# Performance work log

Measured on AMD Instinct MI355X. Metric: run time of the kernel, lower is better.

The kernel has to match this reference:

```python
import jax, jax.numpy as jnp
import numpy as np

B, L, D = 2, 2048, 2048
H, G, HD = 16, 4, 128
EPS = 1e-6
THETA_BASE = 10000.0


def setup_inputs() -> dict:
    key = jax.random.key(0)
    ks = jax.random.split(key, 5)
    x = jax.random.normal(ks[0], (B, L, D), jnp.float32)
    Wq = jax.random.normal(ks[1], (D, H * HD), jnp.float32) * 0.02
    Wk = jax.random.normal(ks[2], (D, G * HD), jnp.float32) * 0.02
    Wv = jax.random.normal(ks[3], (D, G * HD), jnp.float32) * 0.02
    Wo = jax.random.normal(ks[4], (H * HD, D), jnp.float32) * 0.02
    q_scale = jnp.ones((HD,), jnp.float32)
    k_scale = jnp.ones((HD,), jnp.float32)
    # Well-formed RoPE tables of shape [L, HD] (duplicated-half layout expected by apply_rope)
    inv_freq = 1.0 / (THETA_BASE ** (jnp.arange(0, HD // 2, dtype=jnp.float32) * 2.0 / HD))  # [HD/2]
    angles = jnp.arange(L, dtype=jnp.float32)[:, None] * inv_freq[None, :]  # [L, HD/2]
    angles = jnp.concatenate([angles, angles], axis=1)  # [L, HD]
    cos = jnp.cos(angles)
    sin = jnp.sin(angles)
    # Causal mask: True = masked (matches masked_fill(mask, -inf))
    mask = jnp.triu(jnp.ones((L, L), dtype=bool), k=1)
    return {"x": x, "Wq": Wq, "Wk": Wk, "Wv": Wv, "Wo": Wo,
            "q_scale": q_scale, "k_scale": k_scale, "cos": cos, "sin": sin, "mask": mask}


def _rmsnorm(x, scale):
    var = jnp.mean(x * x, axis=-1, keepdims=True)
    return x * jax.lax.rsqrt(var + EPS) * scale


def _rope(x, cos, sin):
    # x: [B, h, L, HD]; cos/sin: [L, HD]
    hd = x.shape[-1]
    x1, x2 = x[..., : hd // 2], x[..., hd // 2 :]
    rotated = jnp.concatenate([-x2, x1], axis=-1)
    return x * cos[None, None] + rotated * sin[None, None]


def reference(x, Wq, Wk, Wv, Wo, q_scale, k_scale, cos, sin, mask):
    b, l, _ = x.shape
    q = (x @ Wq).reshape(b, l, H, HD).transpose(0, 2, 1, 3)  # [B,H,L,HD]
    k = (x @ Wk).reshape(b, l, G, HD).transpose(0, 2, 1, 3)  # [B,G,L,HD]
    v = (x @ Wv).reshape(b, l, G, HD).transpose(0, 2, 1, 3)
    q = _rmsnorm(q, q_scale)
    k = _rmsnorm(k, k_scale)
    q = _rope(q, cos, sin)
    k = _rope(k, cos, sin)
    gs = H // G
    k = jnp.repeat(k, gs, axis=1)  # [B,H,L,HD]
    v = jnp.repeat(v, gs, axis=1)
    scores = jnp.einsum('bhqd,bhkd->bhqk', q, k)
    scores = jnp.where(mask, -jnp.inf, scores)
    # NB: faithful to the source's unusual scaling by head_dim**2 (not sqrt)
    w = jax.nn.softmax(scores / float(HD ** 2), axis=-1)
    out = jnp.einsum('bhqk,bhkd->bhqd', w, v).transpose(0, 2, 1, 3).reshape(b, l, H * HD)
    return out @ Wo
```

## Files before the change

kernel.cpp:

```cpp
#include <hip/hip_runtime.h>
#include <math.h>

#define SEQ 2048
#define DMODEL 2048
#define NHQ 16
#define NHK 4

typedef __attribute__((ext_vector_type(8))) short short8;
typedef __attribute__((ext_vector_type(4))) float floatx4;

__device__ __forceinline__ unsigned short f2bf(float f) {
  unsigned int u = __builtin_bit_cast(unsigned int, f);
  u += 0x7fffu + ((u >> 16) & 1u);
  return (unsigned short)(u >> 16);
}
__device__ __forceinline__ float bf2f(unsigned short s) {
  unsigned int u = ((unsigned int)s) << 16;
  return __builtin_bit_cast(float, u);
}

__global__ __launch_bounds__(256) void prep(const float* __restrict__ x,
                                            const float* __restrict__ Wq,
                                            const float* __restrict__ Wk,
                                            const float* __restrict__ Wv,
                                            const float* __restrict__ Wo,
                                            unsigned short* __restrict__ x_bf,
                                            unsigned short* __restrict__ wqkv_t,
                                            unsigned short* __restrict__ wo_t) {
  const int z = blockIdx.z;
  const int tx = threadIdx.x, ty = threadIdx.y;
  if (z == 3) {
    const size_t base = ((size_t)(blockIdx.y * 64 + blockIdx.x)) * 2048 + (ty * 32 + tx) * 8;
    const float4 v0 = *(const float4*)(x + base);
    const float4 v1 = *(const float4*)(x + base + 4);
    ushort4 w0, w1;
    w0.x = f2bf(v0.x); w0.y = f2bf(v0.y); w0.z = f2bf(v0.z); w0.w = f2bf(v0.w);
    w1.x = f2bf(v1.x); w1.y = f2bf(v1.y); w1.z = f2bf(v1.z); w1.w = f2bf(v1.w);
    *(ushort4*)(x_bf + base) = w0;
    *(ushort4*)(x_bf + base + 4) = w1;
    return;
  }
  int bx = blockIdx.x;
  const float* in;
  unsigned short* out;
  int C;
  const int R = 2048;
  if (z == 0)      { in = Wq; out = wqkv_t;                          C = 2048; }
  else if (z == 1) { in = Wo; out = wo_t;                            C = 2048; }
  else {
    if (bx < 16)      { in = Wk; out = wqkv_t + (size_t)2048 * 2048; C = 512; }
    else if (bx < 32) { in = Wv; out = wqkv_t + (size_t)2560 * 2048; C = 512; bx -= 16; }
    else return;
  }
  __shared__ float tile[32][33];
  const int c0 = bx * 32, r0 = blockIdx.y * 32;
#pragma unroll
  for (int j = 0; j < 4; ++j)
    tile[ty + j * 8][tx] = in[(size_t)(r0 + ty + j * 8) * C + c0 + tx];
  __syncthreads();
#pragma unroll
  for (int j = 0; j < 4; ++j)
    out[(size_t)(c0 + ty + j * 8) * R + r0 + tx] = f2bf(tile[tx][ty + j * 8]);
}

__global__ __launch_bounds__(256) void gemm_qkv_fused(const unsigned short* __restrict__ A,
                                                      const unsigned short* __restrict__ Bt,
                                                      unsigned short* __restrict__ qout,
                                                      unsigned short* __restrict__ kout,
                                                      unsigned short* __restrict__ vout,
                                                      const float* __restrict__ q_scale,
                                                      const float* __restrict__ k_scale,
                                                      const float* __restrict__ cosb,
                                                      const float* __restrict__ sinb) {
  __shared__ unsigned short smem[128 * 129];
  unsigned short* As = smem;
  unsigned short* Bs = smem + 128 * 32;

  const int tid = threadIdx.x;
  const int wave = tid >> 6;
  const int lane = tid & 63;
  const int bm = blockIdx.y * 128;
  const int bx = blockIdx.x;
  const int bn = bx * 128;
  const int wr = wave >> 1;
  const int wc = wave & 1;
  const int m15 = lane & 15;
  const int quad = lane >> 4;

  floatx4 acc[4][4];
#pragma unroll
  for (int i = 0; i < 4; ++i)
#pragma unroll
    for (int j = 0; j < 4; ++j) acc[i][j] = (floatx4){0.f, 0.f, 0.f, 0.f};

  const int srow = lane >> 2;
  const int scol = (lane & 3) * 8;

  for (int k0 = 0; k0 < 2048; k0 += 32) {
#pragma unroll
    for (int it = 0; it < 2; ++it) {
      const int rowa = wave * 32 + it * 16;
      const unsigned short* ga = A + (size_t)(bm + rowa + srow) * 2048 + k0 + scol;
      const unsigned short* gb = Bt + (size_t)(bn + rowa + srow) * 2048 + k0 + scol;
      __builtin_amdgcn_global_load_lds(
          (const __attribute__((address_space(1))) void*)ga,
          (__attribute__((address_space(3))) void*)&As[rowa * 32], 16, 0, 0);
      __builtin_amdgcn_global_load_lds(
          (const __attribute__((address_space(1))) void*)gb,
          (__attribute__((address_space(3))) void*)&Bs[rowa * 32], 16, 0, 0);
    }
    __syncthreads();

    short8 af[4], bfr[4];
    const unsigned short* pa = &As[(wr * 64 + m15) * 32 + quad * 8];
    const unsigned short* pb = &Bs[(wc * 64 + m15) * 32 + quad * 8];
#pragma unroll
    for (int i = 0; i < 4; ++i) af[i] = *(const short8*)(pa + i * 16 * 32);
#pragma unroll
    for (int j = 0; j < 4; ++j) bfr[j] = *(const short8*)(pb + j * 16 * 32);
#pragma unroll
    for (int i = 0; i < 4; ++i)
#pragma unroll
      for (int j = 0; j < 4; ++j)
        acc[i][j] = __builtin_amdgcn_mfma_f32_16x16x32_bf16(af[i], bfr[j], acc[i][j], 0, 0, 0);
    __syncthreads();
  }

#pragma unroll
  for (int i = 0; i < 4; ++i)
#pragma unroll
    for (int j = 0; j < 4; ++j) {
      const int col = wc * 64 + j * 16 + m15;
#pragma unroll
      for (int reg = 0; reg < 4; ++reg) {
        const int row = wr * 64 + i * 16 + quad * 4 + reg;
        smem[row * 129 + col] = f2bf(acc[i][j][reg]);
      }
    }
  __syncthreads();

  const int t = tid & 63;
  const int wv = tid >> 6;
  const int b = bm >> 11;
  const int l_base = bm & (SEQ - 1);

  if (bx < 20) {
    const float* scale = (bx < NHQ) ? q_scale : k_scale;
    unsigned short* dstbase = (bx < NHQ)
        ? qout + ((size_t)(b * NHQ + bx) * SEQ + l_base) * 128
        : kout + ((size_t)(b * NHK + (bx - NHQ)) * SEQ + l_base) * 128;
    const float sc0 = scale[t];
    const float sc1 = scale[t + 64];
#pragma unroll 4
    for (int rr = 0; rr < 32; ++rr) {
      const int row = wv * 32 + rr;
      const float v0 = bf2f(smem[row * 129 + t]);
      const float v1 = bf2f(smem[row * 129 + t + 64]);
      float ss = v0 * v0 + v1 * v1;
#pragma unroll
      for (int m = 1; m < 64; m <<= 1) ss += __shfl_xor(ss, m);
      const float r = rsqrtf(ss * (1.0f / 128.0f) + 1e-6f);
      const int l = l_base + row;
      const float c0 = cosb[(size_t)l * 128 + t];
      const float s0 = sinb[(size_t)l * 128 + t];
      const float c1 = cosb[(size_t)l * 128 + t + 64];
      const float s1 = sinb[(size_t)l * 128 + t + 64];
      const float a0 = v0 * r * sc0;
      const float a1 = v1 * r * sc1;
      unsigned short* dst = dstbase + (size_t)row * 128;
      dst[t]      = f2bf(a0 * c0 - a1 * s0);
      dst[t + 64] = f2bf(a1 * c1 + a0 * s1);
    }
  } else {
    const int g = bx - 20;
    unsigned short* vbase = vout + (size_t)(b * NHK + g) * 128 * SEQ + l_base;
#pragma unroll 4
    for (int dd = 0; dd < 32; ++dd) {
      const int d = wv * 32 + dd;
      unsigned short* dst = vbase + (size_t)d * SEQ;
      dst[t]      = smem[t * 129 + d];
      dst[t + 64] = smem[(t + 64) * 129 + d];
    }
  }
}

__global__ __launch_bounds__(256) void gemm_bf16_f32(const unsigned short* __restrict__ A,
                                                     const unsigned short* __restrict__ Bt,
                                                     float* __restrict__ C,
                                                     int M, int N, int K) {
  __shared__ unsigned short As[128 * 32];
  __shared__ unsigned short Bs[128 * 32];
  const int tid = threadIdx.x;
  const int wave = tid >> 6;
  const int lane = tid & 63;
  const int bm = blockIdx.y * 128;
  const int bn = blockIdx.x * 128;
  const int wr = wave >> 1;
  const int wc = wave & 1;
  const int m15 = lane & 15;
  const int quad = lane >> 4;

  floatx4 acc[4][4];
#pragma unroll
  for (int i = 0; i < 4; ++i)
#pragma unroll
    for (int j = 0; j < 4; ++j) acc[i][j] = (floatx4){0.f, 0.f, 0.f, 0.f};

  const int srow = lane >> 2;
  const int scol = (lane & 3) * 8;

  for (int k0 = 0; k0 < K; k0 += 32) {
#pragma unroll
    for (int it = 0; it < 2; ++it) {
      const int rowa = wave * 32 + it * 16;
      const unsigned short* ga = A + (size_t)(bm + rowa + srow) * K + k0 + scol;
      const unsigned short* gb = Bt + (size_t)(bn + rowa + srow) * K + k0 + scol;
      __builtin_amdgcn_global_load_lds(
          (const __attribute__((address_space(1))) void*)ga,
          (__attribute__((address_space(3))) void*)&As[rowa * 32], 16, 0, 0);
      __builtin_amdgcn_global_load_lds(
          (const __attribute__((address_space(1))) void*)gb,
          (__attribute__((address_space(3))) void*)&Bs[rowa * 32], 16, 0, 0);
    }
    __syncthreads();

    short8 af[4], bfr[4];
    const unsigned short* pa = &As[(wr * 64 + m15) * 32 + quad * 8];
    const unsigned short* pb = &Bs[(wc * 64 + m15) * 32 + quad * 8];
#pragma unroll
    for (int i = 0; i < 4; ++i) af[i] = *(const short8*)(pa + i * 16 * 32);
#pragma unroll
    for (int j = 0; j < 4; ++j) bfr[j] = *(const short8*)(pb + j * 16 * 32);
#pragma unroll
    for (int i = 0; i < 4; ++i)
#pragma unroll
      for (int j = 0; j < 4; ++j)
        acc[i][j] = __builtin_amdgcn_mfma_f32_16x16x32_bf16(af[i], bfr[j], acc[i][j], 0, 0, 0);
    __syncthreads();
  }

#pragma unroll
  for (int i = 0; i < 4; ++i)
#pragma unroll
    for (int j = 0; j < 4; ++j) {
      const int col = bn + wc * 64 + j * 16 + m15;
#pragma unroll
      for (int reg = 0; reg < 4; ++reg) {
        const int row = bm + wr * 64 + i * 16 + quad * 4 + reg;
        C[(size_t)row * N + col] = acc[i][j][reg];
      }
    }
}

__global__ __launch_bounds__(256, 4) void attn_mfma(const unsigned short* __restrict__ qb,
                                                    const unsigned short* __restrict__ kb,
                                                    const unsigned short* __restrict__ vtb,
                                                    unsigned short* __restrict__ o) {
  __shared__ unsigned short Ks[64 * 128];
  __shared__ unsigned short Vs[128 * 64];
  unsigned short* Ps = Ks;

  const int tid = threadIdx.x;
  const int wave = tid >> 6;
  const int lane = tid & 63;
  const int m15 = lane & 15;
  const int quad = lane >> 4;
  const int bh = blockIdx.x;
  const int b = bh >> 4;
  const int h = bh & 15;
  const int g = h >> 2;
  const int q0 = ((int)gridDim.y - 1 - (int)blockIdx.y) * 64;

  const unsigned short* qhead = qb + (size_t)bh * SEQ * 128;
  const unsigned short* khead = kb + (size_t)(b * NHK + g) * SEQ * 128;
  const unsigned short* vthead = vtb + (size_t)(b * NHK + g) * 128 * SEQ;

  short8 qf[4];
  {
    const unsigned short* qp = qhead + (size_t)(q0 + wave * 16 + m15) * 128 + quad * 8;
#pragma unroll
    for (int ks = 0; ks < 4; ++ks) qf[ks] = *(const short8*)(qp + ks * 32);
  }

  floatx4 acc_o[8];
#pragma unroll
  for (int n = 0; n < 8; ++n) acc_o[n] = (floatx4){0.f, 0.f, 0.f, 0.f};
  float l_lane[4] = {0.f, 0.f, 0.f, 0.f};
  const float inv_scale = 1.0f / 16384.0f;

  for (int j0 = 0; j0 <= q0; j0 += 64) {
#pragma unroll
    for (int t = 0; t < 4; ++t) {
      const int r = wave * 16 + t * 4 + (lane >> 4);
      const int cg = (lane & 15) ^ (r & 15);
      const unsigned short* src = khead + (size_t)(j0 + r) * 128 + cg * 8;
      __builtin_amdgcn_global_load_lds(
          (const __attribute__((address_space(1))) void*)src,
          (__attribute__((address_space(3))) void*)&Ks[(wave * 16 + t * 4) * 128], 16, 0, 0);
    }
#pragma unroll
    for (int t = 0; t < 4; ++t) {
      const int d = wave * 32 + t * 8 + (lane >> 3);
      const int cg = (lane & 7) ^ (d & 7);
      const unsigned short* src = vthead + (size_t)d * SEQ + j0 + cg * 8;
      __builtin_amdgcn_global_load_lds(
          (const __attribute__((address_space(1))) void*)src,
          (__attribute__((address_space(3))) void*)&Vs[(wave * 32 + t * 8) * 64], 16, 0, 0);
    }
    __syncthreads();

    floatx4 acc_s[4];
#pragma unroll
    for (int n = 0; n < 4; ++n) acc_s[n] = (floatx4){0.f, 0.f, 0.f, 0.f};
#pragma unroll
    for (int ks = 0; ks < 4; ++ks) {
#pragma unroll
      for (int n = 0; n < 4; ++n) {
        const short8 bfrag = *(const short8*)&Ks[(n * 16 + m15) * 128 + (((ks * 4 + quad) ^ m15) * 8)];
        acc_s[n] = __builtin_amdgcn_mfma_f32_16x16x32_bf16(qf[ks], bfrag, acc_s[n], 0, 0, 0);
      }
    }
    __syncthreads();

    if (j0 == q0) {
      const int row_g = wave * 16 + quad * 4;
#pragma unroll
      for (int n = 0; n < 4; ++n) {
        const int col = n * 16 + m15;
#pragma unroll
        for (int rg = 0; rg < 4; ++rg) {
          float p = (col > row_g + rg) ? 0.0f : __expf(acc_s[n][rg] * inv_scale);
          l_lane[rg] += p;
          Ps[(wave * 16 + quad * 4 + rg) * 72 + n * 16 + m15] = f2bf(p);
        }
      }
    } else {
#pragma unroll
      for (int n = 0; n < 4; ++n) {
#pragma unroll
        for (int rg = 0; rg < 4; ++rg) {
          const float p = __expf(acc_s[n][rg] * inv_scale);
          l_lane[rg] += p;
          Ps[(wave * 16 + quad * 4 + rg) * 72 + n * 16 + m15] = f2bf(p);
        }
      }
    }

#pragma unroll
    for (int kk = 0; kk < 2; ++kk) {
      const short8 a = *(const short8*)&Ps[(wave * 16 + m15) * 72 + kk * 32 + quad * 8];
#pragma unroll
      for (int n = 0; n < 8; ++n) {
        const short8 bfrag = *(const short8*)&Vs[(n * 16 + m15) * 64 + (((kk * 4 + quad) ^ (m15 & 7)) * 8)];
        acc_o[n] = __builtin_amdgcn_mfma_f32_16x16x32_bf16(a, bfrag, acc_o[n], 0, 0, 0);
      }
    }
    __syncthreads();
  }

#pragma unroll
  for (int rg = 0; rg < 4; ++rg) {
    float l = l_lane[rg];
    l += __shfl_xor(l, 1);
    l += __shfl_xor(l, 2);
    l += __shfl_xor(l, 4);
    l += __shfl_xor(l, 8);
    const float invl = 1.0f / l;
    const size_t row = (size_t)(b * SEQ + q0 + wave * 16 + quad * 4 + rg);
#pragma unroll
    for (int n = 0; n < 8; ++n)
      o[row * DMODEL + h * 128 + n * 16 + m15] = f2bf(acc_o[n][rg] * invl);
  }
}

extern "C" void kernel_launch(void* const* d_in, const int* in_sizes, int n_in,
                              void* d_out, int out_size, void* d_ws, size_t ws_size,
                              hipStream_t stream) {
  const float* x       = (const float*)d_in[0];
  const float* Wq      = (const float*)d_in[1];
  const float* Wk      = (const float*)d_in[2];
  const float* Wv      = (const float*)d_in[3];
  const float* Wo      = (const float*)d_in[4];
  const float* q_scale = (const float*)d_in[5];
  const float* k_scale = (const float*)d_in[6];
  const float* cosb    = (const float*)d_in[7];
  const float* sinb    = (const float*)d_in[8];
  float* out = (float*)d_out;

  char* w = (char*)d_ws;
  unsigned short* x_bf    = (unsigned short*)w;
  unsigned short* wqkv_t  = (unsigned short*)(w + 16777216);
  unsigned short* q_bf    = (unsigned short*)(w + 29360128);
  unsigned short* k_bf    = (unsigned short*)(w + 46137344);
  unsigned short* vt      = (unsigned short*)(w + 50331648);
  unsigned short* wo_t    = (unsigned short*)(w + 54525952);
  unsigned short* attn_bf = (unsigned short*)(w + 62914560);

  prep<<<dim3(64, 64, 4), dim3(32, 8), 0, stream>>>(x, Wq, Wk, Wv, Wo, x_bf, wqkv_t, wo_t);

  gemm_qkv_fused<<<dim3(24, 32), 256, 0, stream>>>(x_bf, wqkv_t, q_bf, k_bf, vt,
                                                   q_scale, k_scale, cosb, sinb);

  attn_mfma<<<dim3(2 * NHQ, SEQ / 64), 256, 0, stream>>>(q_bf, k_bf, vt, attn_bf);
  gemm_bf16_f32<<<dim3(2048 / 128, 4096 / 128), 256, 0, stream>>>(
      attn_bf, wo_t, out, 4096, 2048, 2048);
}
```

Baseline: 322.4 us.

## Double-buffer LDS staging in GEMMs and widen prep conversion/transpose stores

Both bf16 GEMM kernels now use two LDS buffers, so the global-to-LDS load for the next K slice is issued before the MFMAs on the current slice, overlapping memory latency with compute. The prep kernel handles twice as many elements per block, with 16-byte vector stores for the x conversion and for the weight transposes (64-row tiles). The price is more LDS per block in gemm_bf16_f32 and a correctness dependence on the async loads finishing before the barrier. The load into buffer 1 is issued before reading buffer 0, and each buffer is only reused after a sync.

```diff
diff --git a/kernel.cpp b/kernel.cpp
--- a/kernel.cpp
+++ b/kernel.cpp
@@ -7,6 +7,7 @@
 #define NHK 4
 
 typedef __attribute__((ext_vector_type(8))) short short8;
+typedef __attribute__((ext_vector_type(8))) unsigned short ushort8;
 typedef __attribute__((ext_vector_type(4))) float floatx4;
 
 __device__ __forceinline__ unsigned short f2bf(float f) {
@@ -29,15 +30,20 @@
                                             unsigned short* __restrict__ wo_t) {
   const int z = blockIdx.z;
   const int tx = threadIdx.x, ty = threadIdx.y;
+  const int tid = ty * 32 + tx;
   if (z == 3) {
-    const size_t base = ((size_t)(blockIdx.y * 64 + blockIdx.x)) * 2048 + (ty * 32 + tx) * 8;
+    const size_t base = ((size_t)(blockIdx.y * 64 + blockIdx.x)) * 4096 + (size_t)tid * 16;
     const float4 v0 = *(const float4*)(x + base);
     const float4 v1 = *(const float4*)(x + base + 4);
-    ushort4 w0, w1;
-    w0.x = f2bf(v0.x); w0.y = f2bf(v0.y); w0.z = f2bf(v0.z); w0.w = f2bf(v0.w);
-    w1.x = f2bf(v1.x); w1.y = f2bf(v1.y); w1.z = f2bf(v1.z); w1.w = f2bf(v1.w);
-    *(ushort4*)(x_bf + base) = w0;
-    *(ushort4*)(x_bf + base + 4) = w1;
+    const float4 v2 = *(const float4*)(x + base + 8);
+    const float4 v3 = *(const float4*)(x + base + 12);
+    ushort8 w0, w1;
+    w0[0] = f2bf(v0.x); w0[1] = f2bf(v0.y); w0[2] = f2bf(v0.z); w0[3] = f2bf(v0.w);
+    w0[4] = f2bf(v1.x); w0[5] = f2bf(v1.y); w0[6] = f2bf(v1.z); w0[7] = f2bf(v1.w);
+    w1[0] = f2bf(v2.x); w1[1] = f2bf(v2.y); w1[2] = f2bf(v2.z); w1[3] = f2bf(v2.w);
+    w1[4] = f2bf(v3.x); w1[5] = f2bf(v3.y); w1[6] = f2bf(v3.z); w1[7] = f2bf(v3.w);
+    *(ushort8*)(x_bf + base) = w0;
+    *(ushort8*)(x_bf + base + 8) = w1;
     return;
   }
   int bx = blockIdx.x;
@@ -52,15 +58,54 @@
     else if (bx < 32) { in = Wv; out = wqkv_t + (size_t)2560 * 2048; C = 512; bx -= 16; }
     else return;
   }
-  __shared__ float tile[32][33];
-  const int c0 = bx * 32, r0 = blockIdx.y * 32;
-#pragma unroll
-  for (int j = 0; j < 4; ++j)
-    tile[ty + j * 8][tx] = in[(size_t)(r0 + ty + j * 8) * C + c0 + tx];
+  __shared__ float tile[32][65];
+  const int c0 = bx * 32, r0 = blockIdx.y * 64;
+#pragma unroll
+  for (int j = 0; j < 8; ++j)
+    tile[tx][ty + j * 8] = in[(size_t)(r0 + ty + j * 8) * C + c0 + tx];
   __syncthreads();
-#pragma unroll
-  for (int j = 0; j < 4; ++j)
-    out[(size_t)(c0 + ty + j * 8) * R + r0 + tx] = f2bf(tile[tx][ty + j * 8]);
+  const int c = tid >> 3;
+  const int l8 = tid & 7;
+  ushort8 w;
+#pragma unroll
+  for (int u = 0; u < 8; ++u) w[u] = f2bf(tile[c][l8 * 8 + u]);
+  *(ushort8*)(out + (size_t)(c0 + c) * R + r0 + l8 * 8) = w;
+}
+
+__device__ __forceinline__ void stage_tile(const unsigned short* __restrict__ A,
+                                           const unsigned short* __restrict__ Bt,
+                                           unsigned short* As, unsigned short* Bs,
+                                           int bm, int bn, int K, int k0,
+                                           int wave, int srow, int scol) {
+#pragma unroll
+  for (int it = 0; it < 2; ++it) {
+    const int rowa = wave * 32 + it * 16;
+    const unsigned short* ga = A + (size_t)(bm + rowa + srow) * K + k0 + scol;
+    const unsigned short* gb = Bt + (size_t)(bn + rowa + srow) * K + k0 + scol;
+    __builtin_amdgcn_global_load_lds(
+        (const __attribute__((address_space(1))) void*)ga,
+        (__attribute__((address_space(3))) void*)&As[rowa * 32], 16, 0, 0);
+    __builtin_amdgcn_global_load_lds(
+        (const __attribute__((address_space(1))) void*)gb,
+        (__attribute__((address_space(3))) void*)&Bs[rowa * 32], 16, 0, 0);
+  }
+}
+
+__device__ __forceinline__ void mfma_tile(const unsigned short* As, const unsigned short* Bs,
+                                          floatx4 (&acc)[4][4],
+                                          int wr, int wc, int m15, int quad) {
+  short8 af[4], bfr[4];
+  const unsigned short* pa = &As[(wr * 64 + m15) * 32 + quad * 8];
+  const unsigned short* pb = &Bs[(wc * 64 + m15) * 32 + quad * 8];
+#pragma unroll
+  for (int i = 0; i < 4; ++i) af[i] = *(const short8*)(pa + i * 16 * 32);
+#pragma unroll
+  for (int j = 0; j < 4; ++j) bfr[j] = *(const short8*)(pb + j * 16 * 32);
+#pragma unroll
+  for (int i = 0; i < 4; ++i)
+#pragma unroll
+    for (int j = 0; j < 4; ++j)
+      acc[i][j] = __builtin_amdgcn_mfma_f32_16x16x32_bf16(af[i], bfr[j], acc[i][j], 0, 0, 0);
 }
 
 __global__ __launch_bounds__(256) void gemm_qkv_fused(const unsigned short* __restrict__ A,
@@ -73,8 +118,10 @@
                                                       const float* __restrict__ cosb,
                                                       const float* __restrict__ sinb) {
   __shared__ unsigned short smem[128 * 129];
-  unsigned short* As = smem;
-  unsigned short* Bs = smem + 128 * 32;
+  unsigned short* As0 = smem;
+  unsigned short* Bs0 = smem + 4096;
+  unsigned short* As1 = smem + 8192;
+  unsigned short* Bs1 = smem + 12288;
 
   const int tid = threadIdx.x;
   const int wave = tid >> 6;
@@ -96,33 +143,16 @@
   const int srow = lane >> 2;
   const int scol = (lane & 3) * 8;
 
-  for (int k0 = 0; k0 < 2048; k0 += 32) {
-#pragma unroll
-    for (int it = 0; it < 2; ++it) {
-      const int rowa = wave * 32 + it * 16;
-      const unsigned short* ga = A + (size_t)(bm + rowa + srow) * 2048 + k0 + scol;
-      const unsigned short* gb = Bt + (size_t)(bn + rowa + srow) * 2048 + k0 + scol;
-      __builtin_amdgcn_global_load_lds(
-          (const __attribute__((address_space(1))) void*)ga,
-          (__attribute__((address_space(3))) void*)&As[rowa * 32], 16, 0, 0);
-      __builtin_amdgcn_global_load_lds(
-          (const __attribute__((address_space(1))) void*)gb,
-          (__attribute__((address_space(3))) void*)&Bs[rowa * 32], 16, 0, 0);
-    }
-    __syncthreads();
-
-    short8 af[4], bfr[4];
-    const unsigned short* pa = &As[(wr * 64 + m15) * 32 + quad * 8];
-    const unsigned short* pb = &Bs[(wc * 64 + m15) * 32 + quad * 8];
-#pragma unroll
-    for (int i = 0; i < 4; ++i) af[i] = *(const short8*)(pa + i * 16 * 32);
-#pragma unroll
-    for (int j = 0; j < 4; ++j) bfr[j] = *(const short8*)(pb + j * 16 * 32);
-#pragma unroll
-    for (int i = 0; i < 4; ++i)
-#pragma unroll
-      for (int j = 0; j < 4; ++j)
-        acc[i][j] = __builtin_amdgcn_mfma_f32_16x16x32_bf16(af[i], bfr[j], acc[i][j], 0, 0, 0);
+  stage_tile(A, Bt, As0, Bs0, bm, bn, 2048, 0, wave, srow, scol);
+  __syncthreads();
+
+  for (int k0 = 0; k0 < 2048; k0 += 64) {
+    stage_tile(A, Bt, As1, Bs1, bm, bn, 2048, k0 + 32, wave, srow, scol);
+    mfma_tile(As0, Bs0, acc, wr, wc, m15, quad);
+    __syncthreads();
+    if (k0 + 64 < 2048)
+      stage_tile(A, Bt, As0, Bs0, bm, bn, 2048, k0 + 64, wave, srow, scol);
+    mfma_tile(As1, Bs1, acc, wr, wc, m15, quad);
     __syncthreads();
   }
 
@@ -188,8 +218,12 @@
                                                      const unsigned short* __restrict__ Bt,
                                                      float* __restrict__ C,
                                                      int M, int N, int K) {
-  __shared__ unsigned short As[128 * 32];
-  __shared__ unsigned short Bs[128 * 32];
+  __shared__ unsigned short smem[4 * 128 * 32];
+  unsigned short* As0 = smem;
+  unsigned short* Bs0 = smem + 4096;
+  unsigned short* As1 = smem + 8192;
+  unsigned short* Bs1 = smem + 12288;
+
   const int tid = threadIdx.x;
   const int wave = tid >> 6;
   const int lane = tid & 63;
@@ -209,33 +243,16 @@
   const int srow = lane >> 2;
   const int scol = (lane & 3) * 8;
 
-  for (int k0 = 0; k0 < K; k0 += 32) {
-#pragma unroll
-    for (int it = 0; it < 2; ++it) {
-      const int rowa = wave * 32 + it * 16;
-      const unsigned short* ga = A + (size_t)(bm + rowa + srow) * K + k0 + scol;
-      const unsigned short* gb = Bt + (size_t)(bn + rowa + srow) * K + k0 + scol;
-      __builtin_amdgcn_global_load_lds(
-          (const __attribute__((address_space(1))) void*)ga,
-          (__attribute__((address_space(3))) void*)&As[rowa * 32], 16, 0, 0);
-      __builtin_amdgcn_global_load_lds(
-          (const __attribute__((address_space(1))) void*)gb,
-          (__attribute__((address_space(3))) void*)&Bs[rowa * 32], 16, 0, 0);
-    }
-    __syncthreads();
-
-    short8 af[4], bfr[4];
-    const unsigned short* pa = &As[(wr * 64 + m15) * 32 + quad * 8];
-    const unsigned short* pb = &Bs[(wc * 64 + m15) * 32 + quad * 8];
-#pragma unroll
-    for (int i = 0; i < 4; ++i) af[i] = *(const short8*)(pa + i * 16 * 32);
-#pragma unroll
-    for (int j = 0; j < 4; ++j) bfr[j] = *(const short8*)(pb + j * 16 * 32);
-#pragma unroll
-    for (int i = 0; i < 4; ++i)
-#pragma unroll
-      for (int j = 0; j < 4; ++j)
-        acc[i][j] = __builtin_amdgcn_mfma_f32_16x16x32_bf16(af[i], bfr[j], acc[i][j], 0, 0, 0);
+  stage_tile(A, Bt, As0, Bs0, bm, bn, K, 0, wave, srow, scol);
+  __syncthreads();
+
+  for (int k0 = 0; k0 < K; k0 += 64) {
+    stage_tile(A, Bt, As1, Bs1, bm, bn, K, k0 + 32, wave, srow, scol);
+    mfma_tile(As0, Bs0, acc, wr, wc, m15, quad);
+    __syncthreads();
+    if (k0 + 64 < K)
+      stage_tile(A, Bt, As0, Bs0, bm, bn, K, k0 + 64, wave, srow, scol);
+    mfma_tile(As1, Bs1, acc, wr, wc, m15, quad);
     __syncthreads();
   }
 
@@ -396,7 +413,7 @@
   unsigned short* wo_t    = (unsigned short*)(w + 54525952);
   unsigned short* attn_bf = (unsigned short*)(w + 62914560);
 
-  prep<<<dim3(64, 64, 4), dim3(32, 8), 0, stream>>>(x, Wq, Wk, Wv, Wo, x_bf, wqkv_t, wo_t);
+  prep<<<dim3(64, 32, 4), dim3(32, 8), 0, stream>>>(x, Wq, Wk, Wv, Wo, x_bf, wqkv_t, wo_t);
 
   gemm_qkv_fused<<<dim3(24, 32), 256, 0, stream>>>(x_bf, wqkv_t, q_bf, k_bf, vt,
                                                    q_scale, k_scale, cosb, sinb);
```

After: 313.3 us. 2.8% less time.
